# Optimization experiments

Hardware: AMD Instinct MI355X
Metric: run time of the kernel (lower is better)

## Reference

```python
import jax, jax.numpy as jnp
import numpy as np

EPS = 1e-05


def _convert(t):
    # torch: squeeze(0).permute(2,1,0): [1,C,H,W] -> [W,H,C]
    return jnp.transpose(t[0], (2, 1, 0))


def _histogram(t):
    # t: [W,H,C]; m: per-channel mean; h: [C, W*H]; ch: CxC covariance + eps*I
    m = t.mean(axis=(0, 1))
    c = t.shape[2]
    h = jnp.transpose(t - m, (2, 0, 1)).reshape(c, -1)
    ch = h @ h.T / h.shape[1] + EPS * jnp.eye(c, dtype=t.dtype)
    return m, h, ch


def _pca(c):
    # evec @ diag(sqrt(evals)) @ evec.T, with nan->0 on the sqrt
    w, v = jnp.linalg.eigh(c)
    e = jnp.sqrt(w)
    e = jnp.where(jnp.isnan(e), jnp.zeros_like(e), e)
    return (v * e[None, :]) @ v.T


def setup_inputs() -> dict:
    key = jax.random.key(0)
    k1, k2 = jax.random.split(key)
    shape = (1, 3, 2048, 2048)
    return {
        "input": jax.random.normal(k1, shape, dtype=jnp.float32),
        "source_tensor": jax.random.normal(k2, shape, dtype=jnp.float32),
    }


def reference(input, source_tensor):
    tgt = _convert(input)          # [W,H,C]
    src = _convert(source_tensor)  # [Ws,Hs,C]
    _, t, ct = _histogram(tgt)
    ms, _, cs = _histogram(src)
    # mode == 'pca': mt = pca(cs) @ inv(pca(ct)) @ t
    transform = _pca(cs) @ jnp.linalg.inv(_pca(ct))  # [C,C]
    mt = transform @ t                               # [C, W*H]
    w, h, c = tgt.shape
    matched = jnp.transpose(mt.reshape(c, w, h), (1, 2, 0)) + ms  # [W,H,C]
    # convert back: permute(2,1,0).unsqueeze(0) -> [1,C,H,W]
    return jnp.transpose(matched, (2, 1, 0))[None]
```

## Files before the change

kernel.cpp:

```cpp
#include <hip/hip_runtime.h>

#define EPS 1e-5
constexpr int BLOCK = 256;
constexpr int SBLOCKS = 512;

__global__ void stats_kernel(const float* __restrict__ in0,
                             const float* __restrict__ in1,
                             double* __restrict__ partials, int n4) {
    const float4* base = (const float4*)(blockIdx.y == 0 ? in0 : in1);
    double s0 = 0, s1 = 0, s2 = 0;
    double q00 = 0, q01 = 0, q02 = 0, q11 = 0, q12 = 0, q22 = 0;
    int stride = gridDim.x * blockDim.x;
    for (int i = blockIdx.x * blockDim.x + threadIdx.x; i < n4; i += stride) {
        float4 a = base[i];
        float4 b = base[i + n4];
        float4 c = base[i + 2 * n4];
#define ACC(f) { double x = (double)a.f, y = (double)b.f, z = (double)c.f;      \
        s0 += x; s1 += y; s2 += z;                                              \
        q00 = fma(x, x, q00); q01 = fma(x, y, q01); q02 = fma(x, z, q02);       \
        q11 = fma(y, y, q11); q12 = fma(y, z, q12); q22 = fma(z, z, q22); }
        ACC(x) ACC(y) ACC(z) ACC(w)
#undef ACC
    }
    double v[9] = {s0, s1, s2, q00, q01, q02, q11, q12, q22};
    int lane = threadIdx.x & 63;
    int wid  = threadIdx.x >> 6;
    __shared__ double sh[BLOCK / 64][9];
#pragma unroll
    for (int j = 0; j < 9; ++j) {
        double t = v[j];
#pragma unroll
        for (int o = 32; o > 0; o >>= 1) t += __shfl_down(t, o, 64);
        if (lane == 0) sh[wid][j] = t;
    }
    __syncthreads();
    if (threadIdx.x == 0) {
        double* out = partials + (blockIdx.y * SBLOCKS + blockIdx.x) * 9;
#pragma unroll
        for (int j = 0; j < 9; ++j) {
            double t = 0;
#pragma unroll
            for (int wv = 0; wv < BLOCK / 64; ++wv) t += sh[wv][j];
            out[j] = t;
        }
    }
}

__device__ void jacobi3(const double Ain[3][3], double w[3], double V[3][3]) {
    double A[3][3];
    for (int i = 0; i < 3; ++i)
        for (int j = 0; j < 3; ++j) {
            A[i][j] = Ain[i][j];
            V[i][j] = (i == j) ? 1.0 : 0.0;
        }
    const int pp[3] = {0, 0, 1};
    const int qq[3] = {1, 2, 2};
    for (int sweep = 0; sweep < 50; ++sweep) {
        double off = A[0][1]*A[0][1] + A[0][2]*A[0][2] + A[1][2]*A[1][2];
        if (off < 1e-28) break;
        for (int r3 = 0; r3 < 3; ++r3) {
            int p = pp[r3], q = qq[r3];
            double apq = A[p][q];
            if (apq == 0.0) continue;
            double theta = (A[q][q] - A[p][p]) / (2.0 * apq);
            double t = ((theta >= 0.0) ? 1.0 : -1.0) /
                       (fabs(theta) + sqrt(theta * theta + 1.0));
            double c = 1.0 / sqrt(t * t + 1.0);
            double s = t * c;
            A[p][p] -= t * apq;
            A[q][q] += t * apq;
            A[p][q] = A[q][p] = 0.0;
            int r = 3 - p - q;
            double arp = A[r][p], arq = A[r][q];
            A[r][p] = A[p][r] = c * arp - s * arq;
            A[r][q] = A[q][r] = s * arp + c * arq;
            for (int k = 0; k < 3; ++k) {
                double vkp = V[k][p], vkq = V[k][q];
                V[k][p] = c * vkp - s * vkq;
                V[k][q] = s * vkp + c * vkq;
            }
        }
    }
    w[0] = A[0][0]; w[1] = A[1][1]; w[2] = A[2][2];
}

__device__ void pca_pow(const double w[3], const double V[3][3], bool invert,
                        double P[3][3]) {
    double e[3];
    for (int k = 0; k < 3; ++k) {
        double ek = (w[k] > 0.0) ? sqrt(w[k]) : 0.0;
        if (invert) ek = (ek > 0.0) ? 1.0 / ek : 0.0;
        e[k] = ek;
    }
    for (int i = 0; i < 3; ++i)
        for (int j = 0; j < 3; ++j) {
            double t = 0;
            for (int k = 0; k < 3; ++k) t += V[i][k] * e[k] * V[j][k];
            P[i][j] = t;
        }
}

__global__ void solve_kernel(const double* __restrict__ partials,
                             float* __restrict__ tb, double inv_n) {
    __shared__ double ssum[2][9];
    __shared__ double sh[BLOCK / 64][9];
    int lane = threadIdx.x & 63;
    int wid  = threadIdx.x >> 6;
    for (int img = 0; img < 2; ++img) {
        const double* p0 = partials + (img * SBLOCKS + threadIdx.x) * 9;
        const double* p1 = p0 + BLOCK * 9;
        double v[9];
#pragma unroll
        for (int j = 0; j < 9; ++j) v[j] = p0[j] + p1[j];
#pragma unroll
        for (int j = 0; j < 9; ++j) {
            double t = v[j];
#pragma unroll
            for (int o = 32; o > 0; o >>= 1) t += __shfl_down(t, o, 64);
            if (lane == 0) sh[wid][j] = t;
        }
        __syncthreads();
        if (threadIdx.x == 0) {
#pragma unroll
            for (int j = 0; j < 9; ++j)
                ssum[img][j] = sh[0][j] + sh[1][j] + sh[2][j] + sh[3][j];
        }
        __syncthreads();
    }
    if (threadIdx.x != 0) return;

    double mean[2][3];
    double P[2][3][3];
    for (int im = 0; im < 2; ++im) {
        const double* a = ssum[im];
        double m0 = a[0] * inv_n, m1 = a[1] * inv_n, m2 = a[2] * inv_n;
        mean[im][0] = m0; mean[im][1] = m1; mean[im][2] = m2;
        double C[3][3];
        C[0][0] = a[3] * inv_n - m0 * m0 + EPS;
        C[0][1] = C[1][0] = a[4] * inv_n - m0 * m1;
        C[0][2] = C[2][0] = a[5] * inv_n - m0 * m2;
        C[1][1] = a[6] * inv_n - m1 * m1 + EPS;
        C[1][2] = C[2][1] = a[7] * inv_n - m1 * m2;
        C[2][2] = a[8] * inv_n - m2 * m2 + EPS;
        double w[3], V[3][3];
        jacobi3(C, w, V);
        pca_pow(w, V, im == 0 , P[im]);
    }
    double T[3][3];
    for (int i = 0; i < 3; ++i)
        for (int j = 0; j < 3; ++j) {
            double t = 0;
            for (int k = 0; k < 3; ++k) t += P[1][i][k] * P[0][k][j];
            T[i][j] = t;
        }
    for (int i = 0; i < 3; ++i) {
        double b = mean[1][i];
        for (int k = 0; k < 3; ++k) b -= T[i][k] * mean[0][k];
        tb[3 * i + 0] = (float)T[i][0];
        tb[3 * i + 1] = (float)T[i][1];
        tb[3 * i + 2] = (float)T[i][2];
        tb[9 + i] = (float)b;
    }
}

__global__ void apply_kernel(const float* __restrict__ in,
                             const float* __restrict__ tb,
                             float* __restrict__ out, int n4) {
    float t00 = tb[0], t01 = tb[1], t02 = tb[2];
    float t10 = tb[3], t11 = tb[4], t12 = tb[5];
    float t20 = tb[6], t21 = tb[7], t22 = tb[8];
    float b0 = tb[9], b1 = tb[10], b2 = tb[11];
    const float4* a = (const float4*)in;
    float4* o = (float4*)out;
    int stride = gridDim.x * blockDim.x;
    for (int i = blockIdx.x * blockDim.x + threadIdx.x; i < n4; i += stride) {
        float4 x = a[i];
        float4 y = a[i + n4];
        float4 z = a[i + 2 * n4];
        float4 r0, r1, r2;
#define AP(f) r0.f = fmaf(t00, x.f, fmaf(t01, y.f, fmaf(t02, z.f, b0)));       \
              r1.f = fmaf(t10, x.f, fmaf(t11, y.f, fmaf(t12, z.f, b1)));       \
              r2.f = fmaf(t20, x.f, fmaf(t21, y.f, fmaf(t22, z.f, b2)));
        AP(x) AP(y) AP(z) AP(w)
#undef AP
        o[i] = r0;
        o[i + n4] = r1;
        o[i + 2 * n4] = r2;
    }
}

extern "C" void kernel_launch(void* const* d_in, const int* in_sizes, int n_in,
                              void* d_out, int out_size, void* d_ws, size_t ws_size,
                              hipStream_t stream) {
    const float* in0 = (const float*)d_in[0];
    const float* in1 = (const float*)d_in[1];
    float* out = (float*)d_out;
    int total = in_sizes[0];
    int n = total / 3;
    int n4 = n / 4;

    double* partials = (double*)d_ws;
    float* tb = (float*)((char*)d_ws + 2 * SBLOCKS * 9 * sizeof(double));

    dim3 sgrid(SBLOCKS, 2);
    stats_kernel<<<sgrid, BLOCK, 0, stream>>>(in0, in1, partials, n4);
    solve_kernel<<<1, BLOCK, 0, stream>>>(partials, tb, 1.0 / (double)n);
    apply_kernel<<<2048, BLOCK, 0, stream>>>(in0, tb, out, n4);
}
```

Before: 55.36 us.

## Fuse stats, solve and apply into one cooperative kernel with grid syncs

Replaces the three launches (stats, solve, apply) with a single cooperative kernel that uses grid-wide syncs between the reduction, the 3x3 eigen solve and the affine apply. The goal is to remove launch gaps and the kernel-boundary drain between stages, while falling back to the old three-kernel path if the cooperative launch fails. It also parallelizes the two eigen solves across two threads and caps the Jacobi sweeps. The risks are grid-sync overhead, a grid limited to co-resident blocks (at most 1024), and the occupancy and API queries now issued on every call.

```diff
diff --git a/kernel.cpp b/kernel.cpp
--- a/kernel.cpp
+++ b/kernel.cpp
@@ -1,50 +1,11 @@
 #include <hip/hip_runtime.h>
+#include <hip/hip_cooperative_groups.h>
+
+namespace cg = cooperative_groups;
 
 #define EPS 1e-5
 constexpr int BLOCK = 256;
 constexpr int SBLOCKS = 512;
-
-__global__ void stats_kernel(const float* __restrict__ in0,
-                             const float* __restrict__ in1,
-                             double* __restrict__ partials, int n4) {
-    const float4* base = (const float4*)(blockIdx.y == 0 ? in0 : in1);
-    double s0 = 0, s1 = 0, s2 = 0;
-    double q00 = 0, q01 = 0, q02 = 0, q11 = 0, q12 = 0, q22 = 0;
-    int stride = gridDim.x * blockDim.x;
-    for (int i = blockIdx.x * blockDim.x + threadIdx.x; i < n4; i += stride) {
-        float4 a = base[i];
-        float4 b = base[i + n4];
-        float4 c = base[i + 2 * n4];
-#define ACC(f) { double x = (double)a.f, y = (double)b.f, z = (double)c.f;      \
-        s0 += x; s1 += y; s2 += z;                                              \
-        q00 = fma(x, x, q00); q01 = fma(x, y, q01); q02 = fma(x, z, q02);       \
-        q11 = fma(y, y, q11); q12 = fma(y, z, q12); q22 = fma(z, z, q22); }
-        ACC(x) ACC(y) ACC(z) ACC(w)
-#undef ACC
-    }
-    double v[9] = {s0, s1, s2, q00, q01, q02, q11, q12, q22};
-    int lane = threadIdx.x & 63;
-    int wid  = threadIdx.x >> 6;
-    __shared__ double sh[BLOCK / 64][9];
-#pragma unroll
-    for (int j = 0; j < 9; ++j) {
-        double t = v[j];
-#pragma unroll
-        for (int o = 32; o > 0; o >>= 1) t += __shfl_down(t, o, 64);
-        if (lane == 0) sh[wid][j] = t;
-    }
-    __syncthreads();
-    if (threadIdx.x == 0) {
-        double* out = partials + (blockIdx.y * SBLOCKS + blockIdx.x) * 9;
-#pragma unroll
-        for (int j = 0; j < 9; ++j) {
-            double t = 0;
-#pragma unroll
-            for (int wv = 0; wv < BLOCK / 64; ++wv) t += sh[wv][j];
-            out[j] = t;
-        }
-    }
-}
 
 __device__ void jacobi3(const double Ain[3][3], double w[3], double V[3][3]) {
     double A[3][3];
@@ -55,7 +16,7 @@
         }
     const int pp[3] = {0, 0, 1};
     const int qq[3] = {1, 2, 2};
-    for (int sweep = 0; sweep < 50; ++sweep) {
+    for (int sweep = 0; sweep < 20; ++sweep) {
         double off = A[0][1]*A[0][1] + A[0][2]*A[0][2] + A[1][2]*A[1][2];
         if (off < 1e-28) break;
         for (int r3 = 0; r3 < 3; ++r3) {
@@ -100,67 +61,240 @@
         }
 }
 
-__global__ void solve_kernel(const double* __restrict__ partials,
-                             float* __restrict__ tb, double inv_n) {
-    __shared__ double ssum[2][9];
-    __shared__ double sh[BLOCK / 64][9];
-    int lane = threadIdx.x & 63;
-    int wid  = threadIdx.x >> 6;
-    for (int img = 0; img < 2; ++img) {
-        const double* p0 = partials + (img * SBLOCKS + threadIdx.x) * 9;
-        const double* p1 = p0 + BLOCK * 9;
-        double v[9];
-#pragma unroll
-        for (int j = 0; j < 9; ++j) v[j] = p0[j] + p1[j];
-#pragma unroll
-        for (int j = 0; j < 9; ++j) {
-            double t = v[j];
-#pragma unroll
-            for (int o = 32; o > 0; o >>= 1) t += __shfl_down(t, o, 64);
-            if (lane == 0) sh[wid][j] = t;
-        }
-        __syncthreads();
-        if (threadIdx.x == 0) {
-#pragma unroll
-            for (int j = 0; j < 9; ++j)
-                ssum[img][j] = sh[0][j] + sh[1][j] + sh[2][j] + sh[3][j];
-        }
-        __syncthreads();
-    }
-    if (threadIdx.x != 0) return;
-
-    double mean[2][3];
-    double P[2][3][3];
-    for (int im = 0; im < 2; ++im) {
-        const double* a = ssum[im];
-        double m0 = a[0] * inv_n, m1 = a[1] * inv_n, m2 = a[2] * inv_n;
-        mean[im][0] = m0; mean[im][1] = m1; mean[im][2] = m2;
-        double C[3][3];
-        C[0][0] = a[3] * inv_n - m0 * m0 + EPS;
-        C[0][1] = C[1][0] = a[4] * inv_n - m0 * m1;
-        C[0][2] = C[2][0] = a[5] * inv_n - m0 * m2;
-        C[1][1] = a[6] * inv_n - m1 * m1 + EPS;
-        C[1][2] = C[2][1] = a[7] * inv_n - m1 * m2;
-        C[2][2] = a[8] * inv_n - m2 * m2 + EPS;
-        double w[3], V[3][3];
-        jacobi3(C, w, V);
-        pca_pow(w, V, im == 0 , P[im]);
-    }
+__device__ void solve_one(const double* a, double inv_n, bool invert,
+                          double P[3][3], double mean[3]) {
+    double m0 = a[0] * inv_n, m1 = a[1] * inv_n, m2 = a[2] * inv_n;
+    mean[0] = m0; mean[1] = m1; mean[2] = m2;
+    double C[3][3];
+    C[0][0] = a[3] * inv_n - m0 * m0 + EPS;
+    C[0][1] = C[1][0] = a[4] * inv_n - m0 * m1;
+    C[0][2] = C[2][0] = a[5] * inv_n - m0 * m2;
+    C[1][1] = a[6] * inv_n - m1 * m1 + EPS;
+    C[1][2] = C[2][1] = a[7] * inv_n - m1 * m2;
+    C[2][2] = a[8] * inv_n - m2 * m2 + EPS;
+    double w[3], V[3][3];
+    jacobi3(C, w, V);
+    pca_pow(w, V, invert, P);
+}
+
+__device__ void combine_tb(const double Pt[3][3], const double Ps[3][3],
+                           const double mt[3], const double ms[3],
+                           float* tb) {
     double T[3][3];
     for (int i = 0; i < 3; ++i)
         for (int j = 0; j < 3; ++j) {
             double t = 0;
-            for (int k = 0; k < 3; ++k) t += P[1][i][k] * P[0][k][j];
+            for (int k = 0; k < 3; ++k) t += Ps[i][k] * Pt[k][j];
             T[i][j] = t;
         }
     for (int i = 0; i < 3; ++i) {
-        double b = mean[1][i];
-        for (int k = 0; k < 3; ++k) b -= T[i][k] * mean[0][k];
+        double b = ms[i];
+        for (int k = 0; k < 3; ++k) b -= T[i][k] * mt[k];
         tb[3 * i + 0] = (float)T[i][0];
         tb[3 * i + 1] = (float)T[i][1];
         tb[3 * i + 2] = (float)T[i][2];
         tb[9 + i] = (float)b;
     }
+}
+
+__global__ __launch_bounds__(BLOCK, 4)
+void fused_kernel(const float* __restrict__ in0,
+                  const float* __restrict__ in1,
+                  float* __restrict__ out,
+                  double* __restrict__ partials,
+                  float* __restrict__ tb,
+                  int n4, double inv_n) {
+    cg::grid_group grid = cg::this_grid();
+    const int bid = blockIdx.x;
+    const int tid = threadIdx.x;
+    const int lane = tid & 63;
+    const int wid  = tid >> 6;
+    const int half = gridDim.x >> 1;
+    __shared__ double sh[BLOCK / 64][9];
+
+    {
+        const int img = (bid >= half) ? 1 : 0;
+        const float4* base = (const float4*)(img ? in1 : in0);
+        const int b = bid - img * half;
+        double s0 = 0, s1 = 0, s2 = 0;
+        double q00 = 0, q01 = 0, q02 = 0, q11 = 0, q12 = 0, q22 = 0;
+        const int stride = half * BLOCK;
+        for (int i = b * BLOCK + tid; i < n4; i += stride) {
+            float4 a = base[i];
+            float4 bb = base[i + n4];
+            float4 c = base[i + 2 * n4];
+#define ACC(f) { double x = (double)a.f, y = (double)bb.f, z = (double)c.f;     \
+            s0 += x; s1 += y; s2 += z;                                          \
+            q00 = fma(x, x, q00); q01 = fma(x, y, q01); q02 = fma(x, z, q02);   \
+            q11 = fma(y, y, q11); q12 = fma(y, z, q12); q22 = fma(z, z, q22); }
+            ACC(x) ACC(y) ACC(z) ACC(w)
+#undef ACC
+        }
+        double v[9] = {s0, s1, s2, q00, q01, q02, q11, q12, q22};
+#pragma unroll
+        for (int j = 0; j < 9; ++j) {
+            double t = v[j];
+#pragma unroll
+            for (int o = 32; o > 0; o >>= 1) t += __shfl_down(t, o, 64);
+            if (lane == 0) sh[wid][j] = t;
+        }
+        __syncthreads();
+        if (tid == 0) {
+            double* outp = partials + bid * 9;
+#pragma unroll
+            for (int j = 0; j < 9; ++j)
+                outp[j] = sh[0][j] + sh[1][j] + sh[2][j] + sh[3][j];
+        }
+    }
+    __threadfence();
+    grid.sync();
+
+    if (bid == 0) {
+        __shared__ double ssum[2][9];
+        __shared__ double sP[2][3][3];
+        __shared__ double sMean[2][3];
+        for (int img = 0; img < 2; ++img) {
+            double v[9] = {0, 0, 0, 0, 0, 0, 0, 0, 0};
+            for (int s = tid; s < half; s += BLOCK) {
+                const double* p = partials + (img * half + s) * 9;
+#pragma unroll
+                for (int j = 0; j < 9; ++j) v[j] += p[j];
+            }
+#pragma unroll
+            for (int j = 0; j < 9; ++j) {
+                double t = v[j];
+#pragma unroll
+                for (int o = 32; o > 0; o >>= 1) t += __shfl_down(t, o, 64);
+                if (lane == 0) sh[wid][j] = t;
+            }
+            __syncthreads();
+            if (tid == 0) {
+#pragma unroll
+                for (int j = 0; j < 9; ++j)
+                    ssum[img][j] = sh[0][j] + sh[1][j] + sh[2][j] + sh[3][j];
+            }
+            __syncthreads();
+        }
+        if (tid < 2) {
+            double P[3][3], mean[3];
+            solve_one(ssum[tid], inv_n, tid == 0, P, mean);
+            for (int i = 0; i < 3; ++i) {
+                sMean[tid][i] = mean[i];
+                for (int j = 0; j < 3; ++j) sP[tid][i][j] = P[i][j];
+            }
+        }
+        __syncthreads();
+        if (tid == 0) {
+            combine_tb(sP[0], sP[1], sMean[0], sMean[1], tb);
+            __threadfence();
+        }
+    }
+    grid.sync();
+
+    {
+        const float t00 = tb[0], t01 = tb[1], t02 = tb[2];
+        const float t10 = tb[3], t11 = tb[4], t12 = tb[5];
+        const float t20 = tb[6], t21 = tb[7], t22 = tb[8];
+        const float b0 = tb[9], b1 = tb[10], b2 = tb[11];
+        const float4* a = (const float4*)in0;
+        float4* o = (float4*)out;
+        const int stride = gridDim.x * BLOCK;
+        for (int i = bid * BLOCK + tid; i < n4; i += stride) {
+            float4 x = a[i];
+            float4 y = a[i + n4];
+            float4 z = a[i + 2 * n4];
+            float4 r0, r1, r2;
+#define AP(f) r0.f = fmaf(t00, x.f, fmaf(t01, y.f, fmaf(t02, z.f, b0)));       \
+              r1.f = fmaf(t10, x.f, fmaf(t11, y.f, fmaf(t12, z.f, b1)));       \
+              r2.f = fmaf(t20, x.f, fmaf(t21, y.f, fmaf(t22, z.f, b2)));
+            AP(x) AP(y) AP(z) AP(w)
+#undef AP
+            o[i] = r0;
+            o[i + n4] = r1;
+            o[i + 2 * n4] = r2;
+        }
+    }
+}
+
+__global__ void stats_kernel(const float* __restrict__ in0,
+                             const float* __restrict__ in1,
+                             double* __restrict__ partials, int n4) {
+    const float4* base = (const float4*)(blockIdx.y == 0 ? in0 : in1);
+    double s0 = 0, s1 = 0, s2 = 0;
+    double q00 = 0, q01 = 0, q02 = 0, q11 = 0, q12 = 0, q22 = 0;
+    int stride = gridDim.x * blockDim.x;
+    for (int i = blockIdx.x * blockDim.x + threadIdx.x; i < n4; i += stride) {
+        float4 a = base[i];
+        float4 b = base[i + n4];
+        float4 c = base[i + 2 * n4];
+#define ACC(f) { double x = (double)a.f, y = (double)b.f, z = (double)c.f;      \
+        s0 += x; s1 += y; s2 += z;                                              \
+        q00 = fma(x, x, q00); q01 = fma(x, y, q01); q02 = fma(x, z, q02);       \
+        q11 = fma(y, y, q11); q12 = fma(y, z, q12); q22 = fma(z, z, q22); }
+        ACC(x) ACC(y) ACC(z) ACC(w)
+#undef ACC
+    }
+    double v[9] = {s0, s1, s2, q00, q01, q02, q11, q12, q22};
+    int lane = threadIdx.x & 63;
+    int wid  = threadIdx.x >> 6;
+    __shared__ double sh[BLOCK / 64][9];
+#pragma unroll
+    for (int j = 0; j < 9; ++j) {
+        double t = v[j];
+#pragma unroll
+        for (int o = 32; o > 0; o >>= 1) t += __shfl_down(t, o, 64);
+        if (lane == 0) sh[wid][j] = t;
+    }
+    __syncthreads();
+    if (threadIdx.x == 0) {
+        double* out = partials + (blockIdx.y * SBLOCKS + blockIdx.x) * 9;
+#pragma unroll
+        for (int j = 0; j < 9; ++j)
+            out[j] = sh[0][j] + sh[1][j] + sh[2][j] + sh[3][j];
+    }
+}
+
+__global__ void solve_kernel(const double* __restrict__ partials,
+                             float* __restrict__ tb, double inv_n) {
+    __shared__ double ssum[2][9];
+    __shared__ double sP[2][3][3];
+    __shared__ double sMean[2][3];
+    __shared__ double sh[BLOCK / 64][9];
+    int tid = threadIdx.x;
+    int lane = tid & 63;
+    int wid  = tid >> 6;
+    for (int img = 0; img < 2; ++img) {
+        double v[9] = {0, 0, 0, 0, 0, 0, 0, 0, 0};
+        for (int s = tid; s < SBLOCKS; s += BLOCK) {
+            const double* p = partials + (img * SBLOCKS + s) * 9;
+#pragma unroll
+            for (int j = 0; j < 9; ++j) v[j] += p[j];
+        }
+#pragma unroll
+        for (int j = 0; j < 9; ++j) {
+            double t = v[j];
+#pragma unroll
+            for (int o = 32; o > 0; o >>= 1) t += __shfl_down(t, o, 64);
+            if (lane == 0) sh[wid][j] = t;
+        }
+        __syncthreads();
+        if (tid == 0) {
+#pragma unroll
+            for (int j = 0; j < 9; ++j)
+                ssum[img][j] = sh[0][j] + sh[1][j] + sh[2][j] + sh[3][j];
+        }
+        __syncthreads();
+    }
+    if (tid < 2) {
+        double P[3][3], mean[3];
+        solve_one(ssum[tid], inv_n, tid == 0, P, mean);
+        for (int i = 0; i < 3; ++i) {
+            sMean[tid][i] = mean[i];
+            for (int j = 0; j < 3; ++j) sP[tid][i][j] = P[i][j];
+        }
+    }
+    __syncthreads();
+    if (tid == 0) combine_tb(sP[0], sP[1], sMean[0], sMean[1], tb);
 }
 
 __global__ void apply_kernel(const float* __restrict__ in,
@@ -200,10 +334,39 @@
     int n4 = n / 4;
 
     double* partials = (double*)d_ws;
-    float* tb = (float*)((char*)d_ws + 2 * SBLOCKS * 9 * sizeof(double));
-
-    dim3 sgrid(SBLOCKS, 2);
-    stats_kernel<<<sgrid, BLOCK, 0, stream>>>(in0, in1, partials, n4);
-    solve_kernel<<<1, BLOCK, 0, stream>>>(partials, tb, 1.0 / (double)n);
-    apply_kernel<<<2048, BLOCK, 0, stream>>>(in0, tb, out, n4);
-}
+    float* tb = (float*)((char*)d_ws + 80 * 1024);
+    double inv_n = 1.0 / (double)n;
+
+    bool coop_ok = false;
+    int maxBlocksPerCU = 0;
+    if (hipOccupancyMaxActiveBlocksPerMultiprocessor(
+            &maxBlocksPerCU, fused_kernel, BLOCK, 0) == hipSuccess &&
+        maxBlocksPerCU > 0) {
+        int dev = 0;
+        hipGetDevice(&dev);
+        int numCU = 0;
+        if (hipDeviceGetAttribute(&numCU, hipDeviceAttributeMultiprocessorCount,
+                                  dev) != hipSuccess || numCU <= 0)
+            numCU = 256;
+        long g = (long)maxBlocksPerCU * (long)numCU;
+        if (g > 1024) g = 1024;
+        g &= ~1L;
+        if (g >= 2) {
+            int grid = (int)g;
+            void* args[] = {(void*)&in0, (void*)&in1, (void*)&out,
+                            (void*)&partials, (void*)&tb,
+                            (void*)&n4, (void*)&inv_n};
+            if (hipLaunchCooperativeKernel((void*)fused_kernel, dim3(grid),
+                                           dim3(BLOCK), args, 0,
+                                           stream) == hipSuccess)
+                coop_ok = true;
+        }
+    }
+
+    if (!coop_ok) {
+        dim3 sgrid(SBLOCKS, 2);
+        stats_kernel<<<sgrid, BLOCK, 0, stream>>>(in0, in1, partials, n4);
+        solve_kernel<<<1, BLOCK, 0, stream>>>(partials, tb, inv_n);
+        apply_kernel<<<2048, BLOCK, 0, stream>>>(in0, tb, out, n4);
+    }
+}
```

After: 181.5 us. +227.9%, slower.

## Fuse stats and solve kernels via last-block atomic counter

Applied to the files above, without the earlier changes.

Merges the statistics reduction and the 3x3 eigen solve into one kernel: each block writes its partial sums, and the last block to finish (found with an atomic counter) reduces all partials and computes the transform. The stats grid is halved to 256 blocks per image, the two eigen solves run on separate threads, and the Jacobi sweep cap is lowered. This removes one kernel launch and its gap, but adds a memset launch to reset the counter, a grid-wide threadfence, and a serial tail in a single block.

```diff
diff --git a/kernel.cpp b/kernel.cpp
--- a/kernel.cpp
+++ b/kernel.cpp
@@ -2,49 +2,8 @@
 
 #define EPS 1e-5
 constexpr int BLOCK = 256;
-constexpr int SBLOCKS = 512;
-
-__global__ void stats_kernel(const float* __restrict__ in0,
-                             const float* __restrict__ in1,
-                             double* __restrict__ partials, int n4) {
-    const float4* base = (const float4*)(blockIdx.y == 0 ? in0 : in1);
-    double s0 = 0, s1 = 0, s2 = 0;
-    double q00 = 0, q01 = 0, q02 = 0, q11 = 0, q12 = 0, q22 = 0;
-    int stride = gridDim.x * blockDim.x;
-    for (int i = blockIdx.x * blockDim.x + threadIdx.x; i < n4; i += stride) {
-        float4 a = base[i];
-        float4 b = base[i + n4];
-        float4 c = base[i + 2 * n4];
-#define ACC(f) { double x = (double)a.f, y = (double)b.f, z = (double)c.f;      \
-        s0 += x; s1 += y; s2 += z;                                              \
-        q00 = fma(x, x, q00); q01 = fma(x, y, q01); q02 = fma(x, z, q02);       \
-        q11 = fma(y, y, q11); q12 = fma(y, z, q12); q22 = fma(z, z, q22); }
-        ACC(x) ACC(y) ACC(z) ACC(w)
-#undef ACC
-    }
-    double v[9] = {s0, s1, s2, q00, q01, q02, q11, q12, q22};
-    int lane = threadIdx.x & 63;
-    int wid  = threadIdx.x >> 6;
-    __shared__ double sh[BLOCK / 64][9];
-#pragma unroll
-    for (int j = 0; j < 9; ++j) {
-        double t = v[j];
-#pragma unroll
-        for (int o = 32; o > 0; o >>= 1) t += __shfl_down(t, o, 64);
-        if (lane == 0) sh[wid][j] = t;
-    }
-    __syncthreads();
-    if (threadIdx.x == 0) {
-        double* out = partials + (blockIdx.y * SBLOCKS + blockIdx.x) * 9;
-#pragma unroll
-        for (int j = 0; j < 9; ++j) {
-            double t = 0;
-#pragma unroll
-            for (int wv = 0; wv < BLOCK / 64; ++wv) t += sh[wv][j];
-            out[j] = t;
-        }
-    }
-}
+constexpr int SBLOCKS = 256;
+constexpr int TOTAL_STATS = SBLOCKS * 2;
 
 __device__ void jacobi3(const double Ain[3][3], double w[3], double V[3][3]) {
     double A[3][3];
@@ -55,7 +14,7 @@
         }
     const int pp[3] = {0, 0, 1};
     const int qq[3] = {1, 2, 2};
-    for (int sweep = 0; sweep < 50; ++sweep) {
+    for (int sweep = 0; sweep < 20; ++sweep) {
         double off = A[0][1]*A[0][1] + A[0][2]*A[0][2] + A[1][2]*A[1][2];
         if (off < 1e-28) break;
         for (int r3 = 0; r3 < 3; ++r3) {
@@ -100,67 +59,131 @@
         }
 }
 
-__global__ void solve_kernel(const double* __restrict__ partials,
-                             float* __restrict__ tb, double inv_n) {
-    __shared__ double ssum[2][9];
-    __shared__ double sh[BLOCK / 64][9];
-    int lane = threadIdx.x & 63;
-    int wid  = threadIdx.x >> 6;
-    for (int img = 0; img < 2; ++img) {
-        const double* p0 = partials + (img * SBLOCKS + threadIdx.x) * 9;
-        const double* p1 = p0 + BLOCK * 9;
-        double v[9];
-#pragma unroll
-        for (int j = 0; j < 9; ++j) v[j] = p0[j] + p1[j];
-#pragma unroll
-        for (int j = 0; j < 9; ++j) {
-            double t = v[j];
-#pragma unroll
-            for (int o = 32; o > 0; o >>= 1) t += __shfl_down(t, o, 64);
-            if (lane == 0) sh[wid][j] = t;
-        }
-        __syncthreads();
-        if (threadIdx.x == 0) {
-#pragma unroll
-            for (int j = 0; j < 9; ++j)
-                ssum[img][j] = sh[0][j] + sh[1][j] + sh[2][j] + sh[3][j];
-        }
-        __syncthreads();
-    }
-    if (threadIdx.x != 0) return;
-
-    double mean[2][3];
-    double P[2][3][3];
-    for (int im = 0; im < 2; ++im) {
-        const double* a = ssum[im];
-        double m0 = a[0] * inv_n, m1 = a[1] * inv_n, m2 = a[2] * inv_n;
-        mean[im][0] = m0; mean[im][1] = m1; mean[im][2] = m2;
-        double C[3][3];
-        C[0][0] = a[3] * inv_n - m0 * m0 + EPS;
-        C[0][1] = C[1][0] = a[4] * inv_n - m0 * m1;
-        C[0][2] = C[2][0] = a[5] * inv_n - m0 * m2;
-        C[1][1] = a[6] * inv_n - m1 * m1 + EPS;
-        C[1][2] = C[2][1] = a[7] * inv_n - m1 * m2;
-        C[2][2] = a[8] * inv_n - m2 * m2 + EPS;
-        double w[3], V[3][3];
-        jacobi3(C, w, V);
-        pca_pow(w, V, im == 0 , P[im]);
-    }
+__device__ void solve_one(const double* a, double inv_n, bool invert,
+                          double P[3][3], double mean[3]) {
+    double m0 = a[0] * inv_n, m1 = a[1] * inv_n, m2 = a[2] * inv_n;
+    mean[0] = m0; mean[1] = m1; mean[2] = m2;
+    double C[3][3];
+    C[0][0] = a[3] * inv_n - m0 * m0 + EPS;
+    C[0][1] = C[1][0] = a[4] * inv_n - m0 * m1;
+    C[0][2] = C[2][0] = a[5] * inv_n - m0 * m2;
+    C[1][1] = a[6] * inv_n - m1 * m1 + EPS;
+    C[1][2] = C[2][1] = a[7] * inv_n - m1 * m2;
+    C[2][2] = a[8] * inv_n - m2 * m2 + EPS;
+    double w[3], V[3][3];
+    jacobi3(C, w, V);
+    pca_pow(w, V, invert, P);
+}
+
+__device__ void combine_tb(const double Pt[3][3], const double Ps[3][3],
+                           const double mt[3], const double ms[3],
+                           float* tb) {
     double T[3][3];
     for (int i = 0; i < 3; ++i)
         for (int j = 0; j < 3; ++j) {
             double t = 0;
-            for (int k = 0; k < 3; ++k) t += P[1][i][k] * P[0][k][j];
+            for (int k = 0; k < 3; ++k) t += Ps[i][k] * Pt[k][j];
             T[i][j] = t;
         }
     for (int i = 0; i < 3; ++i) {
-        double b = mean[1][i];
-        for (int k = 0; k < 3; ++k) b -= T[i][k] * mean[0][k];
+        double b = ms[i];
+        for (int k = 0; k < 3; ++k) b -= T[i][k] * mt[k];
         tb[3 * i + 0] = (float)T[i][0];
         tb[3 * i + 1] = (float)T[i][1];
         tb[3 * i + 2] = (float)T[i][2];
         tb[9 + i] = (float)b;
     }
+}
+
+__global__ void stats_solve_kernel(const float* __restrict__ in0,
+                                   const float* __restrict__ in1,
+                                   double* __restrict__ partials,
+                                   float* __restrict__ tb,
+                                   unsigned* __restrict__ counter,
+                                   int n4, double inv_n) {
+    const int tid = threadIdx.x;
+    const int lane = tid & 63;
+    const int wid  = tid >> 6;
+    const int img = blockIdx.y;
+    __shared__ double sh[BLOCK / 64][9];
+
+    {
+        const float4* base = (const float4*)(img ? in1 : in0);
+        double s0 = 0, s1 = 0, s2 = 0;
+        double q00 = 0, q01 = 0, q02 = 0, q11 = 0, q12 = 0, q22 = 0;
+        const int stride = SBLOCKS * BLOCK;
+        for (int i = blockIdx.x * BLOCK + tid; i < n4; i += stride) {
+            float4 a = base[i];
+            float4 bb = base[i + n4];
+            float4 c = base[i + 2 * n4];
+#define ACC(f) { double x = (double)a.f, y = (double)bb.f, z = (double)c.f;     \
+            s0 += x; s1 += y; s2 += z;                                          \
+            q00 = fma(x, x, q00); q01 = fma(x, y, q01); q02 = fma(x, z, q02);   \
+            q11 = fma(y, y, q11); q12 = fma(y, z, q12); q22 = fma(z, z, q22); }
+            ACC(x) ACC(y) ACC(z) ACC(w)
+#undef ACC
+        }
+        double v[9] = {s0, s1, s2, q00, q01, q02, q11, q12, q22};
+#pragma unroll
+        for (int j = 0; j < 9; ++j) {
+            double t = v[j];
+#pragma unroll
+            for (int o = 32; o > 0; o >>= 1) t += __shfl_down(t, o, 64);
+            if (lane == 0) sh[wid][j] = t;
+        }
+        __syncthreads();
+        if (tid == 0) {
+            double* outp = partials + (img * SBLOCKS + blockIdx.x) * 9;
+#pragma unroll
+            for (int j = 0; j < 9; ++j)
+                outp[j] = sh[0][j] + sh[1][j] + sh[2][j] + sh[3][j];
+        }
+    }
+
+    __threadfence();
+    __shared__ int islast;
+    if (tid == 0) {
+        unsigned old = atomicAdd(counter, 1u);
+        islast = (old == TOTAL_STATS - 1);
+    }
+    __syncthreads();
+    if (!islast) return;
+    __threadfence();
+
+    __shared__ double ssum[2][9];
+    __shared__ double sP[2][3][3];
+    __shared__ double sMean[2][3];
+    for (int im = 0; im < 2; ++im) {
+        const double* p = partials + (im * SBLOCKS + tid) * 9;
+        double v[9];
+#pragma unroll
+        for (int j = 0; j < 9; ++j) v[j] = p[j];
+        __syncthreads();
+#pragma unroll
+        for (int j = 0; j < 9; ++j) {
+            double t = v[j];
+#pragma unroll
+            for (int o = 32; o > 0; o >>= 1) t += __shfl_down(t, o, 64);
+            if (lane == 0) sh[wid][j] = t;
+        }
+        __syncthreads();
+        if (tid == 0) {
+#pragma unroll
+            for (int j = 0; j < 9; ++j)
+                ssum[im][j] = sh[0][j] + sh[1][j] + sh[2][j] + sh[3][j];
+        }
+        __syncthreads();
+    }
+    if (tid < 2) {
+        double P[3][3], mean[3];
+        solve_one(ssum[tid], inv_n, tid == 0, P, mean);
+        for (int i = 0; i < 3; ++i) {
+            sMean[tid][i] = mean[i];
+            for (int j = 0; j < 3; ++j) sP[tid][i][j] = P[i][j];
+        }
+    }
+    __syncthreads();
+    if (tid == 0) combine_tb(sP[0], sP[1], sMean[0], sMean[1], tb);
 }
 
 __global__ void apply_kernel(const float* __restrict__ in,
@@ -200,10 +223,14 @@
     int n4 = n / 4;
 
     double* partials = (double*)d_ws;
-    float* tb = (float*)((char*)d_ws + 2 * SBLOCKS * 9 * sizeof(double));
+    float* tb = (float*)((char*)d_ws + 40960);
+    unsigned* counter = (unsigned*)((char*)d_ws + 41984);
+    double inv_n = 1.0 / (double)n;
+
+    hipMemsetAsync(counter, 0, sizeof(unsigned), stream);
 
     dim3 sgrid(SBLOCKS, 2);
-    stats_kernel<<<sgrid, BLOCK, 0, stream>>>(in0, in1, partials, n4);
-    solve_kernel<<<1, BLOCK, 0, stream>>>(partials, tb, 1.0 / (double)n);
+    stats_solve_kernel<<<sgrid, BLOCK, 0, stream>>>(in0, in1, partials, tb,
+                                                    counter, n4, inv_n);
     apply_kernel<<<2048, BLOCK, 0, stream>>>(in0, tb, out, n4);
 }
```

Result: slower. 89.90 us (+62.4%).
